# Performance work log

Hardware: AMD Instinct MI355X
Metric: run time of the kernel (lower is better)

Reference implementation:

```python
import jax, jax.numpy as jnp
import numpy as np

NUM_LAYERS = 2


def setup_inputs() -> dict:
    key = jax.random.key(0)
    ks = jax.random.split(key, 8)
    B, S, D, H, O, L = 32, 2048, 512, 512, 512, NUM_LAYERS
    stdv = 1.0 / np.sqrt(H)
    u = lambda k, shape: jax.random.uniform(k, shape, jnp.float32, -stdv, stdv)
    return {
        "x": jax.random.normal(ks[0], (B, S, D), jnp.float32),
        "hidden": jnp.zeros((L, B, H), jnp.float32),
        "w_ih": u(ks[1], (L, H, D)),
        "w_hh": u(ks[2], (L, H, H)),
        "b_ih": u(ks[3], (L, H)),
        "b_hh": u(ks[4], (L, H)),
        "w_out": u(ks[5], (O, H)),
        "b_out": u(ks[6], (O,)),
    }


def reference(x, hidden, w_ih, w_hh, b_ih, b_hh, w_out, b_out):
    # x: [B, S, D]; hidden: [L, B, H]
    L = w_ih.shape[0]

    def step(h, x_t):  # h: [L, B, H], x_t: [B, D]
        new_hs = []
        inp = x_t
        for l in range(L):
            h_new = jnp.tanh(inp @ w_ih[l].T + b_ih[l] + h[l] @ w_hh[l].T + b_hh[l])
            new_hs.append(h_new)
            inp = h_new
        return jnp.stack(new_hs), inp  # carry, output of top layer

    xs = jnp.swapaxes(x, 0, 1)  # [S, B, D]
    _, outs = jax.lax.scan(step, hidden, xs)  # outs: [S, B, H]
    rnn_out = jnp.swapaxes(outs, 0, 1)  # [B, S, H]
    return rnn_out @ w_out.T + b_out  # [B, S, O]
```

## Files before the change

### kernel.cpp

```cpp
#include <hip/hip_runtime.h>


typedef short v8s __attribute__((ext_vector_type(8)));
typedef int   v4i __attribute__((ext_vector_type(4)));
typedef float v4f __attribute__((ext_vector_type(4)));

#define B_  32
#define S_  2048
#define DH  512
#define SLOT32 16384

#define BIAS_OFF  0
#define H0_OFF    8192
#define H1_OFF    (H0_OFF + 4 * 65536)
#define WOUT_OFF  (H1_OFF + 4 * 65536)
#define WIH0_OFF  (WOUT_OFF + 524288)

#define PARTA_BYTES (8 * 4 * 64 * 16)
#define PARTB_BYTES (8 * 2 * 4 * 64 * 16)
#define LDS_BYTES   (PARTA_BYTES + PARTB_BYTES)

static __device__ __forceinline__ unsigned short f2bf(float f) {
  unsigned int u = __builtin_bit_cast(unsigned int, f);
  u += 0x7fffu + ((u >> 16) & 1u);
  return (unsigned short)(u >> 16);
}
static __device__ __forceinline__ float bf2f(unsigned short h) {
  return __builtin_bit_cast(float, ((unsigned int)h) << 16);
}
static __device__ __forceinline__ unsigned packh(float f, unsigned ep) {
  unsigned short hv = f2bf(f);
  unsigned short lv = f2bf(f - bf2f(hv));
  return ((unsigned)hv << 16) | ((unsigned)lv & 0xFFF8u) | ep;
}
static __device__ __forceinline__ v8s pack8(float4 f0, float4 f1) {
  v8s r;
  r[0] = (short)f2bf(f0.x); r[1] = (short)f2bf(f0.y);
  r[2] = (short)f2bf(f0.z); r[3] = (short)f2bf(f0.w);
  r[4] = (short)f2bf(f1.x); r[5] = (short)f2bf(f1.y);
  r[6] = (short)f2bf(f1.z); r[7] = (short)f2bf(f1.w);
  return r;
}
static __device__ __forceinline__ float fast_tanh(float v) {
  float c = fminf(15.f, fmaxf(-15.f, v));
  float e = __expf(2.f * c);
  return (e - 1.f) * __builtin_amdgcn_rcpf(e + 1.f);
}

static __device__ __forceinline__ v4i ld16v(const unsigned* p) {
  v4i r;
  asm volatile("global_load_dwordx4 %0, %1, off sc1"
               : "=v"(r) : "v"(p) : "memory");
  return r;
}
static __device__ __forceinline__ float ld4(const void* p) {
  float r;
  asm volatile("global_load_dword %0, %1, off"
               : "=v"(r) : "v"(p) : "memory");
  return r;
}
static __device__ __forceinline__ void st32u(void* p, unsigned v) {
  asm volatile("global_store_dword %0, %1, off sc1"
               :: "v"(p), "v"(v) : "memory");
}
#define WAITN0() do { asm volatile("s_waitcnt vmcnt(0)" ::: "memory"); \
    __builtin_amdgcn_sched_barrier(0); } while (0)

static __device__ __forceinline__ void poll_frag(const unsigned* b, unsigned ep,
                                                 bool* bad, v4i* o0, v4i* o1,
                                                 v4i* o2, v4i* o3) {
  v4i a0, a1, a2, a3;
  int t = 0;
  for (;;) {
    a0 = ld16v(b); a1 = ld16v(b + 4); a2 = ld16v(b + 32); a3 = ld16v(b + 36);
    WAITN0();
    if (*bad) break;
    unsigned d = 0;
    #pragma unroll
    for (int j = 0; j < 4; ++j)
      d |= ((unsigned)a0[j] ^ ep) | ((unsigned)a1[j] ^ ep)
         | ((unsigned)a2[j] ^ ep) | ((unsigned)a3[j] ^ ep);
    if (__all((d & 7u) == 0u)) break;
    if (++t > (1 << 15)) { *bad = true; break; }
  }
  *o0 = a0; *o1 = a1; *o2 = a2; *o3 = a3;
}
static __device__ __forceinline__ void unp(v4i a, v4i b, v8s* hi, v8s* lo) {
  v8s h, l;
  #pragma unroll
  for (int j = 0; j < 4; ++j) {
    unsigned ua = (unsigned)a[j], ub = (unsigned)b[j];
    h[j]     = (short)(ua >> 16);   l[j]     = (short)(ua & 0xFFF8u);
    h[4 + j] = (short)(ub >> 16);   l[4 + j] = (short)(ub & 0xFFF8u);
  }
  *hi = h; *lo = l;
}

__global__ void rnn_init(const float* __restrict__ hidden,
                         const float* __restrict__ b_ih,
                         const float* __restrict__ b_hh,
                         const float* __restrict__ w_out,
                         const float* __restrict__ w_ih,
                         float* __restrict__ bias,
                         unsigned* __restrict__ h0ring,
                         unsigned* __restrict__ h1ring,
                         unsigned short* __restrict__ woutbf,
                         unsigned short* __restrict__ wih0bf) {
  int i = blockIdx.x * blockDim.x + threadIdx.x;
  int nth = gridDim.x * blockDim.x;
  for (int t = i; t < 1024; t += nth) bias[t] = b_ih[t] + b_hh[t];
  for (int t = i; t < 2 * B_ * DH; t += nth) {
    int l = t >> 14;
    int off = t & 16383;
    unsigned* ring = l ? h1ring : h0ring;
    ring[3 * SLOT32 + off] = packh(hidden[t], 7u);
  }
  for (int t = i; t < 512 * 512; t += nth) {
    woutbf[t] = f2bf(w_out[t]);
    wih0bf[t] = f2bf(w_ih[t]);
  }
}

__global__ __launch_bounds__(512) void proj64(
    const float* __restrict__ src,
    float* __restrict__ dst,
    const unsigned short* __restrict__ wb,
    const float* __restrict__ bias) {
  __shared__ unsigned short lds[64 * 512];
  const int tid = threadIdx.x;
  const int wid = tid >> 6;
  const int lane = tid & 63;
  const size_t row0 = (size_t)blockIdx.x * 64;

  #pragma unroll
  for (int it = 0; it < 8; ++it) {
    int c = it * 512 + tid;
    int row = c >> 6;
    int col8 = c & 63;
    const float4* s4 = (const float4*)(src + (row0 + row) * DH + col8 * 8);
    float4 f0 = s4[0], f1 = s4[1];
    v8s t = pack8(f0, f1);
    int byteoff = row * 1024 + ((col8 * 16) ^ ((row & 7) << 4));
    *(v8s*)((char*)lds + byteoff) = t;
  }
  __syncthreads();

  const int l15 = lane & 15;
  const int kq = (lane >> 4) * 8;

  for (int nt = wid; nt < 32; nt += 8) {
    v4f acc[4];
    #pragma unroll
    for (int mt = 0; mt < 4; ++mt) acc[mt] = (v4f){0.f, 0.f, 0.f, 0.f};
    const unsigned short* wr = wb + (size_t)(nt * 16 + l15) * 512;
    #pragma unroll
    for (int ks = 0; ks < 16; ++ks) {
      int kk = ks * 32 + kq;
      v8s bfrag = *(const v8s*)(wr + kk);
      #pragma unroll
      for (int mt = 0; mt < 4; ++mt) {
        int row = mt * 16 + l15;
        int byteoff = row * 1024 + ((kk * 2) ^ ((row & 7) << 4));
        v8s afrag = *(const v8s*)((char*)lds + byteoff);
        acc[mt] = __builtin_amdgcn_mfma_f32_16x16x32_bf16(afrag, bfrag, acc[mt], 0, 0, 0);
      }
    }
    float bo = bias[nt * 16 + l15];
    #pragma unroll
    for (int mt = 0; mt < 4; ++mt)
      #pragma unroll
      for (int r = 0; r < 4; ++r) {
        int row = mt * 16 + (lane >> 4) * 4 + r;
        int col = nt * 16 + l15;
        dst[(row0 + row) * DH + col] = acc[mt][r] + bo;
      }
  }
}

__global__ __launch_bounds__(512) void rnn_fused(
    const float* __restrict__ z0,
    const float* __restrict__ w_ih,
    const float* __restrict__ w_hh,
    const float* __restrict__ bias,
    unsigned* __restrict__ h0ring,
    unsigned* __restrict__ h1ring,
    float* __restrict__ dout) {
  extern __shared__ char smem[];
  v4f* partA = (v4f*)smem;
  v4f* partB = (v4f*)(smem + PARTA_BYTES);

  const int wg = blockIdx.x;
  const int mh = wg >> 3;
  const int fs = wg & 7;

  const int tid = threadIdx.x;
  const int wid = tid >> 6;
  const int lane = tid & 63;
  const int l15 = lane & 15;
  const int kq = (lane >> 4) * 8;
  const int q4 = (lane >> 4) * 4;

  v8s wfrag[3][4][2];
  {
    const float* wsrcs[3] = { w_hh, w_ih + 512 * 512, w_hh + 512 * 512 };
    #pragma unroll
    for (int g = 0; g < 3; ++g)
      #pragma unroll
      for (int n = 0; n < 4; ++n)
        #pragma unroll
        for (int ks = 0; ks < 2; ++ks) {
          const float* srow = wsrcs[g] +
              (size_t)(fs * 64 + n * 16 + l15) * 512 + wid * 64 + ks * 32 + kq;
          wfrag[g][n][ks] = pack8(*(const float4*)srow, *(const float4*)(srow + 4));
        }
  }
  const int nf = wid & 3;
  const float bias1v = bias[512 + fs * 64 + nf * 16 + l15];
  const size_t abase = (size_t)(mh * 16 + l15) * 512 + wid * 64 + kq;
  const int featf = fs * 64 + nf * 16 + l15;

  bool bad = false;

  float zp[4] = {0.f, 0.f, 0.f, 0.f};
  if (wid < 4) {
    #pragma unroll
    for (int r = 0; r < 4; ++r)
      zp[r] = ld4(z0 + ((size_t)(mh * 16 + q4 + r) * S_ + 0) * DH + featf);
  }

  for (int p = 0; p <= S_; ++p) {
    const unsigned ep0 = (p == 0) ? 7u : (unsigned)(((p - 1) >> 2) & 7);
    const unsigned* h0b = h0ring + (size_t)((p + 3) & 3) * SLOT32 + abase;
    v4i A0, A1, A2, A3;
    poll_frag(h0b, ep0, &bad, &A0, &A1, &A2, &A3);
    v8s h0h0, h0l0, h0h1, h0l1;
    unp(A0, A1, &h0h0, &h0l0);
    unp(A2, A3, &h0h1, &h0l1);

    v4f acc0[4];
    #pragma unroll
    for (int n = 0; n < 4; ++n) {
      acc0[n] = (v4f){0.f, 0.f, 0.f, 0.f};
      acc0[n] = __builtin_amdgcn_mfma_f32_16x16x32_bf16(h0h0, wfrag[0][n][0], acc0[n], 0, 0, 0);
      acc0[n] = __builtin_amdgcn_mfma_f32_16x16x32_bf16(h0l0, wfrag[0][n][0], acc0[n], 0, 0, 0);
      acc0[n] = __builtin_amdgcn_mfma_f32_16x16x32_bf16(h0h1, wfrag[0][n][1], acc0[n], 0, 0, 0);
      acc0[n] = __builtin_amdgcn_mfma_f32_16x16x32_bf16(h0l1, wfrag[0][n][1], acc0[n], 0, 0, 0);
      partA[(wid * 4 + n) * 64 + lane] = acc0[n];
    }
    __syncthreads();

    if (wid < 4 && p < S_) {
      v4f s0 = {0.f, 0.f, 0.f, 0.f};
      #pragma unroll
      for (int w = 0; w < 8; ++w) s0 += partA[(w * 4 + nf) * 64 + lane];
      const unsigned ep = (unsigned)((p >> 2) & 7);
      unsigned* dst = h0ring + (size_t)(p & 3) * SLOT32;
      #pragma unroll
      for (int r = 0; r < 4; ++r) {
        float h0v = fast_tanh(zp[r] + s0[r]);
        st32u(dst + (size_t)(mh * 16 + q4 + r) * 512 + featf, packh(h0v, ep));
      }
    }

    v4i B0, B1, B2, B3;
    const unsigned ep1 = (p == 1) ? 7u : (unsigned)(((p - 2) >> 2) & 7);
    const unsigned* h1b = h1ring + (size_t)((p + 2) & 3) * SLOT32 + abase;
    if (p >= 1) {
      B0 = ld16v(h1b); B1 = ld16v(h1b + 4);
      B2 = ld16v(h1b + 32); B3 = ld16v(h1b + 36);
    }

    v4f acc1[4], acc2[4];
    #pragma unroll
    for (int n = 0; n < 4; ++n) {
      acc1[n] = (v4f){0.f, 0.f, 0.f, 0.f};
      acc2[n] = (v4f){0.f, 0.f, 0.f, 0.f};
      acc1[n] = __builtin_amdgcn_mfma_f32_16x16x32_bf16(h0h0, wfrag[1][n][0], acc1[n], 0, 0, 0);
      acc1[n] = __builtin_amdgcn_mfma_f32_16x16x32_bf16(h0l0, wfrag[1][n][0], acc1[n], 0, 0, 0);
      acc1[n] = __builtin_amdgcn_mfma_f32_16x16x32_bf16(h0h1, wfrag[1][n][1], acc1[n], 0, 0, 0);
      acc1[n] = __builtin_amdgcn_mfma_f32_16x16x32_bf16(h0l1, wfrag[1][n][1], acc1[n], 0, 0, 0);
    }

    if (p >= 1) {
      WAITN0();
      unsigned d = 0;
      #pragma unroll
      for (int j = 0; j < 4; ++j)
        d |= ((unsigned)B0[j] ^ ep1) | ((unsigned)B1[j] ^ ep1)
           | ((unsigned)B2[j] ^ ep1) | ((unsigned)B3[j] ^ ep1);
      if (!__all((d & 7u) == 0u))
        poll_frag(h1b, ep1, &bad, &B0, &B1, &B2, &B3);
      v8s h1h0, h1l0, h1h1, h1l1;
      unp(B0, B1, &h1h0, &h1l0);
      unp(B2, B3, &h1h1, &h1l1);
      #pragma unroll
      for (int n = 0; n < 4; ++n) {
        acc2[n] = __builtin_amdgcn_mfma_f32_16x16x32_bf16(h1h0, wfrag[2][n][0], acc2[n], 0, 0, 0);
        acc2[n] = __builtin_amdgcn_mfma_f32_16x16x32_bf16(h1l0, wfrag[2][n][0], acc2[n], 0, 0, 0);
        acc2[n] = __builtin_amdgcn_mfma_f32_16x16x32_bf16(h1h1, wfrag[2][n][1], acc2[n], 0, 0, 0);
        acc2[n] = __builtin_amdgcn_mfma_f32_16x16x32_bf16(h1l1, wfrag[2][n][1], acc2[n], 0, 0, 0);
      }
    }
    #pragma unroll
    for (int n = 0; n < 4; ++n) {
      partB[((wid * 2 + 0) * 4 + n) * 64 + lane] = acc1[n];
      partB[((wid * 2 + 1) * 4 + n) * 64 + lane] = acc2[n];
    }
    __syncthreads();

    if (wid < 4) {
      if (p >= 1) {
        v4f s1 = {0.f, 0.f, 0.f, 0.f}, s2 = {0.f, 0.f, 0.f, 0.f};
        #pragma unroll
        for (int w = 0; w < 8; ++w) {
          s1 += partB[((w * 2 + 0) * 4 + nf) * 64 + lane];
          s2 += partB[((w * 2 + 1) * 4 + nf) * 64 + lane];
        }
        const unsigned ep = (unsigned)(((p - 1) >> 2) & 7);
        unsigned* dst = h1ring + (size_t)((p - 1) & 3) * SLOT32;
        #pragma unroll
        for (int r = 0; r < 4; ++r) {
          float h1v = fast_tanh(s1[r] + s2[r] + bias1v);
          st32u(dst + (size_t)(mh * 16 + q4 + r) * 512 + featf, packh(h1v, ep));
          dout[((size_t)(mh * 16 + q4 + r) * S_ + (p - 1)) * DH + featf] = h1v;
        }
      }
      if (p + 1 <= S_) {
        const int pz = (p + 1 < S_) ? (p + 1) : (S_ - 1);
        #pragma unroll
        for (int r = 0; r < 4; ++r)
          zp[r] = ld4(z0 + ((size_t)(mh * 16 + q4 + r) * S_ + pz) * DH + featf);
      }
    }
  }
}

extern "C" void kernel_launch(void* const* d_in, const int* in_sizes, int n_in,
                              void* d_out, int out_size, void* d_ws, size_t ws_size,
                              hipStream_t stream) {
  const float* x      = (const float*)d_in[0];
  const float* hidden = (const float*)d_in[1];
  const float* w_ih   = (const float*)d_in[2];
  const float* w_hh   = (const float*)d_in[3];
  const float* b_ih   = (const float*)d_in[4];
  const float* b_hh   = (const float*)d_in[5];
  const float* w_out  = (const float*)d_in[6];
  const float* b_out  = (const float*)d_in[7];
  float* out = (float*)d_out;

  char* wsb = (char*)d_ws;
  float* bias            = (float*)(wsb + BIAS_OFF);
  unsigned* h0ring       = (unsigned*)(wsb + H0_OFF);
  unsigned* h1ring       = (unsigned*)(wsb + H1_OFF);
  unsigned short* woutbf = (unsigned short*)(wsb + WOUT_OFF);
  unsigned short* wih0bf = (unsigned short*)(wsb + WIH0_OFF);

  rnn_init<<<256, 256, 0, stream>>>(hidden, b_ih, b_hh, w_out, w_ih,
                                    bias, h0ring, h1ring, woutbf, wih0bf);
  proj64<<<(B_ * S_) / 64, 512, 0, stream>>>(x, out, wih0bf, bias);
  rnn_fused<<<16, 512, LDS_BYTES, stream>>>(out, w_ih, w_hh, bias,
                                            h0ring, h1ring, out);
  proj64<<<(B_ * S_) / 64, 512, 0, stream>>>(out, out, woutbf, b_out);
}
```

Measured before the change: 7.701 ms.

## Split recurrent kernel into separate layer-0 and layer-1 workgroup roles

The fused recurrent kernel now launches 32 workgroups instead of 16. Half of them compute only layer 0 and the other half compute only layer 1, so the two layers pipeline across timesteps rather than running serially inside each step. The h rings grow from 4 to 8 slots, and a progress-flag array lets layer-0 workgroups throttle so they never overwrite slots layer 1 has not yet consumed. Per-step LDS partials are double-buffered by step parity. The cost is extra cross-workgroup flag traffic and polling, plus a more delicate synchronisation protocol.

Result: no change. 7.578 ms (-1.6%).

```diff
diff --git a/kernel.cpp b/kernel.cpp
--- a/kernel.cpp
+++ b/kernel.cpp
@@ -8,17 +8,19 @@
 #define B_  32
 #define S_  2048
 #define DH  512
+#define RD  8
+#define RMASK 7
 #define SLOT32 16384
-
-#define BIAS_OFF  0
+#define EPOCH(q) ((unsigned)(((q) >> 3) & 7))
+
+#define PROG_OFF  0
+#define BIAS_OFF  4096
 #define H0_OFF    8192
-#define H1_OFF    (H0_OFF + 4 * 65536)
-#define WOUT_OFF  (H1_OFF + 4 * 65536)
+#define H1_OFF    (H0_OFF + 8 * 65536)
+#define WOUT_OFF  (H1_OFF + 8 * 65536)
 #define WIH0_OFF  (WOUT_OFF + 524288)
 
-#define PARTA_BYTES (8 * 4 * 64 * 16)
-#define PARTB_BYTES (8 * 2 * 4 * 64 * 16)
-#define LDS_BYTES   (PARTA_BYTES + PARTB_BYTES)
+#define LDS_BYTES (2 * 8 * 2 * 4 * 64 * 16)
 
 static __device__ __forceinline__ unsigned short f2bf(float f) {
   unsigned int u = __builtin_bit_cast(unsigned int, f);
@@ -59,9 +61,25 @@
                : "=v"(r) : "v"(p) : "memory");
   return r;
 }
+static __device__ __forceinline__ unsigned ld4u(const void* p) {
+  unsigned r;
+  asm volatile("global_load_dword %0, %1, off sc1"
+               : "=v"(r) : "v"(p) : "memory");
+  return r;
+}
 static __device__ __forceinline__ void st32u(void* p, unsigned v) {
   asm volatile("global_store_dword %0, %1, off sc1"
                :: "v"(p), "v"(v) : "memory");
+}
+static __device__ __forceinline__ void st32m(void* p, unsigned v) {
+  asm volatile("global_store_dword %0, %1, off sc0 sc1"
+               :: "v"(p), "v"(v) : "memory");
+}
+static __device__ __forceinline__ int ld_flag(const int* p) {
+  int r;
+  asm volatile("global_load_dword %0, %1, off sc1\n\ts_waitcnt vmcnt(0)"
+               : "=v"(r) : "v"(p) : "memory");
+  return r;
 }
 #define WAITN0() do { asm volatile("s_waitcnt vmcnt(0)" ::: "memory"); \
     __builtin_amdgcn_sched_barrier(0); } while (0)
@@ -101,6 +119,7 @@
                          const float* __restrict__ b_hh,
                          const float* __restrict__ w_out,
                          const float* __restrict__ w_ih,
+                         unsigned* __restrict__ progress,
                          float* __restrict__ bias,
                          unsigned* __restrict__ h0ring,
                          unsigned* __restrict__ h1ring,
@@ -108,12 +127,13 @@
                          unsigned short* __restrict__ wih0bf) {
   int i = blockIdx.x * blockDim.x + threadIdx.x;
   int nth = gridDim.x * blockDim.x;
+  for (int t = i; t < 1024; t += nth) st32m(progress + t, 0u);
   for (int t = i; t < 1024; t += nth) bias[t] = b_ih[t] + b_hh[t];
   for (int t = i; t < 2 * B_ * DH; t += nth) {
     int l = t >> 14;
     int off = t & 16383;
     unsigned* ring = l ? h1ring : h0ring;
-    ring[3 * SLOT32 + off] = packh(hidden[t], 7u);
+    st32m(ring + (RD - 1) * SLOT32 + off, packh(hidden[t], 7u));
   }
   for (int t = i; t < 512 * 512; t += nth) {
     woutbf[t] = f2bf(w_out[t]);
@@ -184,13 +204,14 @@
     const float* __restrict__ bias,
     unsigned* __restrict__ h0ring,
     unsigned* __restrict__ h1ring,
+    unsigned* __restrict__ progress,
     float* __restrict__ dout) {
   extern __shared__ char smem[];
-  v4f* partA = (v4f*)smem;
-  v4f* partB = (v4f*)(smem + PARTA_BYTES);
+  v4f* part = (v4f*)smem;
 
   const int wg = blockIdx.x;
-  const int mh = wg >> 3;
+  const int role = wg >> 4;
+  const int mh = (wg >> 3) & 1;
   const int fs = wg & 7;
 
   const int tid = threadIdx.x;
@@ -199,137 +220,160 @@
   const int l15 = lane & 15;
   const int kq = (lane >> 4) * 8;
   const int q4 = (lane >> 4) * 4;
-
-  v8s wfrag[3][4][2];
-  {
-    const float* wsrcs[3] = { w_hh, w_ih + 512 * 512, w_hh + 512 * 512 };
-    #pragma unroll
-    for (int g = 0; g < 3; ++g)
-      #pragma unroll
-      for (int n = 0; n < 4; ++n)
-        #pragma unroll
-        for (int ks = 0; ks < 2; ++ks) {
-          const float* srow = wsrcs[g] +
-              (size_t)(fs * 64 + n * 16 + l15) * 512 + wid * 64 + ks * 32 + kq;
-          wfrag[g][n][ks] = pack8(*(const float4*)srow, *(const float4*)(srow + 4));
-        }
-  }
   const int nf = wid & 3;
-  const float bias1v = bias[512 + fs * 64 + nf * 16 + l15];
+
   const size_t abase = (size_t)(mh * 16 + l15) * 512 + wid * 64 + kq;
   const int featf = fs * 64 + nf * 16 + l15;
-
   bool bad = false;
 
-  float zp[4] = {0.f, 0.f, 0.f, 0.f};
-  if (wid < 4) {
+  if (role == 0) {
+    v8s wf[4][2];
     #pragma unroll
-    for (int r = 0; r < 4; ++r)
-      zp[r] = ld4(z0 + ((size_t)(mh * 16 + q4 + r) * S_ + 0) * DH + featf);
-  }
-
-  for (int p = 0; p <= S_; ++p) {
-    const unsigned ep0 = (p == 0) ? 7u : (unsigned)(((p - 1) >> 2) & 7);
-    const unsigned* h0b = h0ring + (size_t)((p + 3) & 3) * SLOT32 + abase;
-    v4i A0, A1, A2, A3;
-    poll_frag(h0b, ep0, &bad, &A0, &A1, &A2, &A3);
-    v8s h0h0, h0l0, h0h1, h0l1;
-    unp(A0, A1, &h0h0, &h0l0);
-    unp(A2, A3, &h0h1, &h0l1);
-
-    v4f acc0[4];
-    #pragma unroll
-    for (int n = 0; n < 4; ++n) {
-      acc0[n] = (v4f){0.f, 0.f, 0.f, 0.f};
-      acc0[n] = __builtin_amdgcn_mfma_f32_16x16x32_bf16(h0h0, wfrag[0][n][0], acc0[n], 0, 0, 0);
-      acc0[n] = __builtin_amdgcn_mfma_f32_16x16x32_bf16(h0l0, wfrag[0][n][0], acc0[n], 0, 0, 0);
-      acc0[n] = __builtin_amdgcn_mfma_f32_16x16x32_bf16(h0h1, wfrag[0][n][1], acc0[n], 0, 0, 0);
-      acc0[n] = __builtin_amdgcn_mfma_f32_16x16x32_bf16(h0l1, wfrag[0][n][1], acc0[n], 0, 0, 0);
-      partA[(wid * 4 + n) * 64 + lane] = acc0[n];
+    for (int n = 0; n < 4; ++n)
+      #pragma unroll
+      for (int ks = 0; ks < 2; ++ks) {
+        const float* srow = w_hh +
+            (size_t)(fs * 64 + n * 16 + l15) * 512 + wid * 64 + ks * 32 + kq;
+        wf[n][ks] = pack8(*(const float4*)srow, *(const float4*)(srow + 4));
+      }
+    const unsigned* pbase = progress + (size_t)(mh * 8 + (lane & 7)) * 64;
+
+    for (int p = 0; p < S_; ++p) {
+      unsigned prog = ld4u(pbase);
+      float zp[4];
+      if (wid < 4) {
+        #pragma unroll
+        for (int r = 0; r < 4; ++r)
+          zp[r] = ld4(z0 + ((size_t)(mh * 16 + q4 + r) * S_ + p) * DH + featf);
+      }
+
+      const unsigned ep0 = (p == 0) ? 7u : EPOCH(p - 1);
+      const unsigned* h0b =
+          h0ring + (size_t)((p + RD - 1) & RMASK) * SLOT32 + abase;
+      v4i A0, A1, A2, A3;
+      poll_frag(h0b, ep0, &bad, &A0, &A1, &A2, &A3);
+
+      asm volatile("" : "+v"(prog));
+      if (p >= 6 && !__all((int)prog >= p - 5)) {
+        int t = 0;
+        for (;;) {
+          int v = ld_flag((const int*)pbase);
+          if (__all(v >= p - 5)) break;
+          if (++t > (1 << 15)) { bad = true; break; }
+        }
+      }
+
+      v8s h0, l0, h1f, l1f;
+      unp(A0, A1, &h0, &l0);
+      unp(A2, A3, &h1f, &l1f);
+      #pragma unroll
+      for (int n = 0; n < 4; ++n) {
+        v4f a = (v4f){0.f, 0.f, 0.f, 0.f};
+        a = __builtin_amdgcn_mfma_f32_16x16x32_bf16(h0,  wf[n][0], a, 0, 0, 0);
+        a = __builtin_amdgcn_mfma_f32_16x16x32_bf16(l0,  wf[n][0], a, 0, 0, 0);
+        a = __builtin_amdgcn_mfma_f32_16x16x32_bf16(h1f, wf[n][1], a, 0, 0, 0);
+        a = __builtin_amdgcn_mfma_f32_16x16x32_bf16(l1f, wf[n][1], a, 0, 0, 0);
+        part[(((p & 1) * 8 + wid) * 4 + n) * 64 + lane] = a;
+      }
+      __syncthreads();
+
+      if (wid < 4) {
+        v4f s = (v4f){0.f, 0.f, 0.f, 0.f};
+        #pragma unroll
+        for (int w = 0; w < 8; ++w)
+          s += part[(((p & 1) * 8 + w) * 4 + nf) * 64 + lane];
+        const unsigned ep = EPOCH(p);
+        unsigned* dst = h0ring + (size_t)(p & RMASK) * SLOT32;
+        #pragma unroll
+        for (int r = 0; r < 4; ++r)
+          st32u(dst + (size_t)(mh * 16 + q4 + r) * 512 + featf,
+                packh(fast_tanh(zp[r] + s[r]), ep));
+      }
     }
-    __syncthreads();
-
-    if (wid < 4 && p < S_) {
-      v4f s0 = {0.f, 0.f, 0.f, 0.f};
-      #pragma unroll
-      for (int w = 0; w < 8; ++w) s0 += partA[(w * 4 + nf) * 64 + lane];
-      const unsigned ep = (unsigned)((p >> 2) & 7);
-      unsigned* dst = h0ring + (size_t)(p & 3) * SLOT32;
-      #pragma unroll
-      for (int r = 0; r < 4; ++r) {
-        float h0v = fast_tanh(zp[r] + s0[r]);
-        st32u(dst + (size_t)(mh * 16 + q4 + r) * 512 + featf, packh(h0v, ep));
-      }
+  } else {
+    v8s wf[2][4][2];
+    {
+      const float* wsrcs[2] = { w_ih + 512 * 512, w_hh + 512 * 512 };
+      #pragma unroll
+      for (int g = 0; g < 2; ++g)
+        #pragma unroll
+        for (int n = 0; n < 4; ++n)
+          #pragma unroll
+          for (int ks = 0; ks < 2; ++ks) {
+            const float* srow = wsrcs[g] +
+                (size_t)(fs * 64 + n * 16 + l15) * 512 + wid * 64 + ks * 32 + kq;
+            wf[g][n][ks] = pack8(*(const float4*)srow, *(const float4*)(srow + 4));
+          }
     }
-
-    v4i B0, B1, B2, B3;
-    const unsigned ep1 = (p == 1) ? 7u : (unsigned)(((p - 2) >> 2) & 7);
-    const unsigned* h1b = h1ring + (size_t)((p + 2) & 3) * SLOT32 + abase;
-    if (p >= 1) {
-      B0 = ld16v(h1b); B1 = ld16v(h1b + 4);
-      B2 = ld16v(h1b + 32); B3 = ld16v(h1b + 36);
-    }
-
-    v4f acc1[4], acc2[4];
-    #pragma unroll
-    for (int n = 0; n < 4; ++n) {
-      acc1[n] = (v4f){0.f, 0.f, 0.f, 0.f};
-      acc2[n] = (v4f){0.f, 0.f, 0.f, 0.f};
-      acc1[n] = __builtin_amdgcn_mfma_f32_16x16x32_bf16(h0h0, wfrag[1][n][0], acc1[n], 0, 0, 0);
-      acc1[n] = __builtin_amdgcn_mfma_f32_16x16x32_bf16(h0l0, wfrag[1][n][0], acc1[n], 0, 0, 0);
-      acc1[n] = __builtin_amdgcn_mfma_f32_16x16x32_bf16(h0h1, wfrag[1][n][1], acc1[n], 0, 0, 0);
-      acc1[n] = __builtin_amdgcn_mfma_f32_16x16x32_bf16(h0l1, wfrag[1][n][1], acc1[n], 0, 0, 0);
-    }
-
-    if (p >= 1) {
-      WAITN0();
-      unsigned d = 0;
-      #pragma unroll
-      for (int j = 0; j < 4; ++j)
-        d |= ((unsigned)B0[j] ^ ep1) | ((unsigned)B1[j] ^ ep1)
-           | ((unsigned)B2[j] ^ ep1) | ((unsigned)B3[j] ^ ep1);
-      if (!__all((d & 7u) == 0u))
-        poll_frag(h1b, ep1, &bad, &B0, &B1, &B2, &B3);
-      v8s h1h0, h1l0, h1h1, h1l1;
-      unp(B0, B1, &h1h0, &h1l0);
-      unp(B2, B3, &h1h1, &h1l1);
+    const float bias1v = bias[512 + fs * 64 + nf * 16 + l15];
+    unsigned* const myprog = progress + (size_t)(mh * 8 + fs) * 64;
+
+    for (int p = 1; p <= S_; ++p) {
+      const unsigned ep1 = (p == 1) ? 7u : EPOCH(p - 2);
+      const unsigned* h1b =
+          h1ring + (size_t)((p + RD - 2) & RMASK) * SLOT32 + abase;
+      v4i B0 = ld16v(h1b), B1 = ld16v(h1b + 4);
+      v4i B2 = ld16v(h1b + 32), B3 = ld16v(h1b + 36);
+
+      const unsigned* h0b = h0ring + (size_t)((p - 1) & RMASK) * SLOT32 + abase;
+      v4i A0, A1, A2, A3;
+      poll_frag(h0b, EPOCH(p - 1), &bad, &A0, &A1, &A2, &A3);
+      if (tid == 0) st32u(myprog, (unsigned)p);
+
+      v8s ah0, al0, ah1, al1;
+      unp(A0, A1, &ah0, &al0);
+      unp(A2, A3, &ah1, &al1);
+      v4f acc1[4], acc2[4];
       #pragma unroll
       for (int n = 0; n < 4; ++n) {
-        acc2[n] = __builtin_amdgcn_mfma_f32_16x16x32_bf16(h1h0, wfrag[2][n][0], acc2[n], 0, 0, 0);
-        acc2[n] = __builtin_amdgcn_mfma_f32_16x16x32_bf16(h1l0, wfrag[2][n][0], acc2[n], 0, 0, 0);
-        acc2[n] = __builtin_amdgcn_mfma_f32_16x16x32_bf16(h1h1, wfrag[2][n][1], acc2[n], 0, 0, 0);
-        acc2[n] = __builtin_amdgcn_mfma_f32_16x16x32_bf16(h1l1, wfrag[2][n][1], acc2[n], 0, 0, 0);
-      }
-    }
-    #pragma unroll
-    for (int n = 0; n < 4; ++n) {
-      partB[((wid * 2 + 0) * 4 + n) * 64 + lane] = acc1[n];
-      partB[((wid * 2 + 1) * 4 + n) * 64 + lane] = acc2[n];
-    }
-    __syncthreads();
-
-    if (wid < 4) {
-      if (p >= 1) {
-        v4f s1 = {0.f, 0.f, 0.f, 0.f}, s2 = {0.f, 0.f, 0.f, 0.f};
+        acc1[n] = (v4f){0.f, 0.f, 0.f, 0.f};
+        acc1[n] = __builtin_amdgcn_mfma_f32_16x16x32_bf16(ah0, wf[0][n][0], acc1[n], 0, 0, 0);
+        acc1[n] = __builtin_amdgcn_mfma_f32_16x16x32_bf16(al0, wf[0][n][0], acc1[n], 0, 0, 0);
+        acc1[n] = __builtin_amdgcn_mfma_f32_16x16x32_bf16(ah1, wf[0][n][1], acc1[n], 0, 0, 0);
+        acc1[n] = __builtin_amdgcn_mfma_f32_16x16x32_bf16(al1, wf[0][n][1], acc1[n], 0, 0, 0);
+      }
+      {
+        unsigned d = 0;
+        #pragma unroll
+        for (int j = 0; j < 4; ++j)
+          d |= ((unsigned)B0[j] ^ ep1) | ((unsigned)B1[j] ^ ep1)
+             | ((unsigned)B2[j] ^ ep1) | ((unsigned)B3[j] ^ ep1);
+        if (!__all((d & 7u) == 0u))
+          poll_frag(h1b, ep1, &bad, &B0, &B1, &B2, &B3);
+      }
+      v8s bh0, bl0, bh1, bl1;
+      unp(B0, B1, &bh0, &bl0);
+      unp(B2, B3, &bh1, &bl1);
+      #pragma unroll
+      for (int n = 0; n < 4; ++n) {
+        acc2[n] = (v4f){0.f, 0.f, 0.f, 0.f};
+        acc2[n] = __builtin_amdgcn_mfma_f32_16x16x32_bf16(bh0, wf[1][n][0], acc2[n], 0, 0, 0);
+        acc2[n] = __builtin_amdgcn_mfma_f32_16x16x32_bf16(bl0, wf[1][n][0], acc2[n], 0, 0, 0);
+        acc2[n] = __builtin_amdgcn_mfma_f32_16x16x32_bf16(bh1, wf[1][n][1], acc2[n], 0, 0, 0);
+        acc2[n] = __builtin_amdgcn_mfma_f32_16x16x32_bf16(bl1, wf[1][n][1], acc2[n], 0, 0, 0);
+      }
+      #pragma unroll
+      for (int n = 0; n < 4; ++n) {
+        part[((((p & 1) * 8 + wid) * 2 + 0) * 4 + n) * 64 + lane] = acc1[n];
+        part[((((p & 1) * 8 + wid) * 2 + 1) * 4 + n) * 64 + lane] = acc2[n];
+      }
+      __syncthreads();
+
+      if (wid < 4) {
+        v4f s1 = (v4f){0.f,0.f,0.f,0.f}, s2 = (v4f){0.f,0.f,0.f,0.f};
         #pragma unroll
         for (int w = 0; w < 8; ++w) {
-          s1 += partB[((w * 2 + 0) * 4 + nf) * 64 + lane];
-          s2 += partB[((w * 2 + 1) * 4 + nf) * 64 + lane];
+          s1 += part[((((p & 1) * 8 + w) * 2 + 0) * 4 + nf) * 64 + lane];
+          s2 += part[((((p & 1) * 8 + w) * 2 + 1) * 4 + nf) * 64 + lane];
         }
-        const unsigned ep = (unsigned)(((p - 1) >> 2) & 7);
-        unsigned* dst = h1ring + (size_t)((p - 1) & 3) * SLOT32;
+        const unsigned ep = EPOCH(p - 1);
+        unsigned* dst = h1ring + (size_t)((p - 1) & RMASK) * SLOT32;
         #pragma unroll
         for (int r = 0; r < 4; ++r) {
           float h1v = fast_tanh(s1[r] + s2[r] + bias1v);
           st32u(dst + (size_t)(mh * 16 + q4 + r) * 512 + featf, packh(h1v, ep));
           dout[((size_t)(mh * 16 + q4 + r) * S_ + (p - 1)) * DH + featf] = h1v;
         }
-      }
-      if (p + 1 <= S_) {
-        const int pz = (p + 1 < S_) ? (p + 1) : (S_ - 1);
-        #pragma unroll
-        for (int r = 0; r < 4; ++r)
-          zp[r] = ld4(z0 + ((size_t)(mh * 16 + q4 + r) * S_ + pz) * DH + featf);
       }
     }
   }
@@ -349,6 +393,7 @@
   float* out = (float*)d_out;
 
   char* wsb = (char*)d_ws;
+  unsigned* progress     = (unsigned*)(wsb + PROG_OFF);
   float* bias            = (float*)(wsb + BIAS_OFF);
   unsigned* h0ring       = (unsigned*)(wsb + H0_OFF);
   unsigned* h1ring       = (unsigned*)(wsb + H1_OFF);
@@ -356,9 +401,10 @@
   unsigned short* wih0bf = (unsigned short*)(wsb + WIH0_OFF);
 
   rnn_init<<<256, 256, 0, stream>>>(hidden, b_ih, b_hh, w_out, w_ih,
-                                    bias, h0ring, h1ring, woutbf, wih0bf);
+                                    progress, bias, h0ring, h1ring,
+                                    woutbf, wih0bf);
   proj64<<<(B_ * S_) / 64, 512, 0, stream>>>(x, out, wih0bf, bias);
-  rnn_fused<<<16, 512, LDS_BYTES, stream>>>(out, w_ih, w_hh, bias,
-                                            h0ring, h1ring, out);
+  rnn_fused<<<32, 512, LDS_BYTES, stream>>>(out, w_ih, w_hh, bias,
+                                            h0ring, h1ring, progress, out);
   proj64<<<(B_ * S_) / 64, 512, 0, stream>>>(out, out, woutbf, b_out);
 }
```
